# Kernel tuning notes

Measured on AMD Instinct MI355X. Metric: run time of the kernel, lower is better.

## Reference

```python
import jax, jax.numpy as jnp
import numpy as np

B, S, D = 1, 2048, 2048
H, HD = 32, 64  # num_heads, head_dim = hidden_size // num_heads


def setup_inputs() -> dict:
    key = jax.random.key(0)
    ks = jax.random.split(key, 7)
    sc = 0.02
    return {
        "hidden_states": jax.random.normal(ks[0], (B, S, D), dtype=jnp.float32),
        "Wq": jax.random.normal(ks[1], (D, D), dtype=jnp.float32) * sc,
        "Wk": jax.random.normal(ks[2], (D, D), dtype=jnp.float32) * sc,
        "Wv": jax.random.normal(ks[3], (D, D), dtype=jnp.float32) * sc,
        "Wf": jax.random.normal(ks[4], (H, D), dtype=jnp.float32) * sc,
        "bf": jax.random.normal(ks[5], (H,), dtype=jnp.float32),
        "Wo": jax.random.normal(ks[6], (D, D), dtype=jnp.float32) * sc,
    }


def reference(hidden_states, Wq, Wk, Wv, Wf, bf, Wo):
    x = hidden_states
    b, s, _ = x.shape
    # projections (nn.Linear: x @ W^T)
    q = (x @ Wq.T).reshape(b, s, H, HD)
    k = (x @ Wk.T).reshape(b, s, H, HD)
    v = (x @ Wv.T).reshape(b, s, H, HD)
    # per-head log forget gates, computed in float32 as in the torch module
    f = jax.nn.log_sigmoid((x @ Wf.T + bf).astype(jnp.float32))  # [b, s, H]
    # cumulative log decay; FoX bias D_ij = F_i - F_j (sum of log gates over (j, i])
    Fcum = jnp.cumsum(f, axis=1)               # [b, s, H]
    Fh = jnp.transpose(Fcum, (0, 2, 1))        # [b, H, s]
    scale = HD ** -0.5
    scores = jnp.einsum('bqhd,bkhd->bhqk', q, k).astype(jnp.float32) * scale
    scores = scores + Fh[:, :, :, None] - Fh[:, :, None, :]
    causal = jnp.tril(jnp.ones((s, s), dtype=bool))
    scores = jnp.where(causal[None, None], scores, -jnp.inf)
    p = jax.nn.softmax(scores, axis=-1).astype(q.dtype)  # [b, H, q, k]
    o = jnp.einsum('bhqk,bkhd->bqhd', p, v).reshape(b, s, D)
    return o @ Wo.T
```

## Files before the change

### kernel.cpp

```cpp
#include <hip/hip_runtime.h>
#include <stdint.h>

#define SEQ 2048
#define DM  2048
#define NH  32
#define HDIM 64

typedef unsigned short u16;
typedef short bf16x8 __attribute__((ext_vector_type(8)));
typedef float f32x4 __attribute__((ext_vector_type(4)));

__device__ __forceinline__ u16 f2bf(float f) {
    union { float f; uint32_t u; } v; v.f = f;
    uint32_t u = v.u;
    uint32_t r = (u + 0x7fffu + ((u >> 16) & 1u)) >> 16;
    return (u16)r;
}

#define GLOAD_LDS16(g, l) __builtin_amdgcn_global_load_lds( \
    (const __attribute__((address_space(1))) uint32_t*)(g), \
    (__attribute__((address_space(3))) uint32_t*)(l), 16, 0, 0)

__global__ __launch_bounds__(256) void convert_bf16(
    const float* __restrict__ X, const float* __restrict__ Wq,
    const float* __restrict__ Wk, const float* __restrict__ Wv,
    const float* __restrict__ Wo,
    u16* __restrict__ Xb, u16* __restrict__ Wqb, u16* __restrict__ Wkb,
    u16* __restrict__ Wvb, u16* __restrict__ Wob)
{
    const int NV = (DM * SEQ) / 4;
    int idx = blockIdx.x * blockDim.x + threadIdx.x;
    int total = NV * 5;
    for (; idx < total; idx += gridDim.x * blockDim.x) {
        int arr = idx / NV, i = idx - arr * NV;
        const float4* s; u16* d;
        switch (arr) {
            case 0:  s = (const float4*)X;  d = Xb;  break;
            case 1:  s = (const float4*)Wq; d = Wqb; break;
            case 2:  s = (const float4*)Wk; d = Wkb; break;
            case 3:  s = (const float4*)Wv; d = Wvb; break;
            default: s = (const float4*)Wo; d = Wob; break;
        }
        float4 v = s[i];
        ushort4 o;
        o.x = f2bf(v.x); o.y = f2bf(v.y); o.z = f2bf(v.z); o.w = f2bf(v.w);
        *(ushort4*)(d + i * 4) = o;
    }
}

__global__ __launch_bounds__(256) void gates_kernel(
    const float* __restrict__ X, const float* __restrict__ Wf,
    float* __restrict__ Fraw)
{
    __shared__ float lX[64 * 68];
    __shared__ float lW[32 * 68];
    int s0 = blockIdx.x * 64;
    int kp = blockIdx.y;
    int tid = threadIdx.x;
    int h = tid & 31, sg = tid >> 5;
    float acc[8] = {0.f,0.f,0.f,0.f,0.f,0.f,0.f,0.f};
    for (int k0 = kp * 512; k0 < kp * 512 + 512; k0 += 64) {
        __syncthreads();
        {
            int r = tid >> 2, seg = tid & 3;
            const float4* src = (const float4*)(X + (size_t)(s0 + r) * DM + k0);
            float4* dst = (float4*)(&lX[r * 68]);
#pragma unroll
            for (int i = 0; i < 4; i++) dst[seg + 4 * i] = src[seg + 4 * i];
#pragma unroll
            for (int j = 0; j < 2; j++) {
                int ii = tid + j * 256;
                int wr_ = ii >> 4, wc_ = ii & 15;
                ((float4*)(&lW[wr_ * 68]))[wc_] =
                    ((const float4*)(Wf + (size_t)wr_ * DM + k0))[wc_];
            }
        }
        __syncthreads();
#pragma unroll
        for (int k4 = 0; k4 < 16; k4++) {
            float4 w = ((const float4*)(&lW[h * 68]))[k4];
#pragma unroll
            for (int i = 0; i < 8; i++) {
                float4 x = ((const float4*)(&lX[(sg + 8 * i) * 68]))[k4];
                acc[i] += x.x * w.x + x.y * w.y + x.z * w.z + x.w * w.w;
            }
        }
    }
#pragma unroll
    for (int i = 0; i < 8; i++)
        atomicAdd(&Fraw[h * SEQ + s0 + sg + 8 * i], acc[i]);
}

__global__ __launch_bounds__(256) void cumsum_kernel(
    float* __restrict__ F, const float* __restrict__ bfp)
{
    __shared__ float lws[4];
    int h = blockIdx.x;
    int tid = threadIdx.x;
    int lane = tid & 63, wv = tid >> 6;
    float bb = bfp[h];
    float4 a = ((const float4*)(F + (size_t)h * SEQ))[tid * 2];
    float4 b2 = ((const float4*)(F + (size_t)h * SEQ))[tid * 2 + 1];
    float v[8] = {a.x, a.y, a.z, a.w, b2.x, b2.y, b2.z, b2.w};
#pragma unroll
    for (int i = 0; i < 8; i++) {
        float g = v[i] + bb;
        v[i] = fminf(g, 0.f) - log1pf(expf(-fabsf(g)));
    }
#pragma unroll
    for (int i = 1; i < 8; i++) v[i] += v[i - 1];
    float tsum = v[7];
    float sc = tsum;
#pragma unroll
    for (int d = 1; d < 64; d <<= 1) {
        float t = __shfl_up(sc, d);
        if (lane >= d) sc += t;
    }
    if (lane == 63) lws[wv] = sc;
    __syncthreads();
    float woff = 0.f;
#pragma unroll
    for (int w2 = 0; w2 < 4; w2++) if (w2 < wv) woff += lws[w2];
    float off = woff + sc - tsum;
#pragma unroll
    for (int i = 0; i < 8; i++) v[i] += off;
    float4 o1 = {v[0], v[1], v[2], v[3]}, o2 = {v[4], v[5], v[6], v[7]};
    ((float4*)(F + (size_t)h * SEQ))[tid * 2] = o1;
    ((float4*)(F + (size_t)h * SEQ))[tid * 2 + 1] = o2;
}

template <bool STOREF32>
__global__ __launch_bounds__(256) void gemm_bt(
    const u16* __restrict__ A,
    const u16* __restrict__ B0, const u16* __restrict__ B1, const u16* __restrict__ B2,
    void* C0, void* C1, void* C2, int M, int N, int K)
{
    __shared__ u16 lA[128 * 32];
    __shared__ u16 lB[128 * 32];
    int z = blockIdx.z;
    const u16* Bm = (z == 0) ? B0 : ((z == 1) ? B1 : B2);
    void* Cm = (z == 0) ? C0 : ((z == 1) ? C1 : C2);
    int m0 = blockIdx.y * 128, n0 = blockIdx.x * 128;
    int tid = threadIdx.x;
    int wave = tid >> 6, lane = tid & 63, ln = lane & 15, quad = lane >> 4;
    int wr = (wave >> 1) * 64, wc = (wave & 1) * 64;

    f32x4 acc[4][4];
#pragma unroll
    for (int i = 0; i < 4; i++)
#pragma unroll
        for (int j = 0; j < 4; j++)
#pragma unroll
            for (int r = 0; r < 4; r++) acc[i][j][r] = 0.f;

    int srow = wave * 32 + (lane >> 2);
    int scol = (lane & 3) * 8;
    const u16* gA0 = &A[(size_t)(m0 + srow) * K + scol];
    const u16* gA1 = &A[(size_t)(m0 + srow + 16) * K + scol];
    const u16* gB0 = &Bm[(size_t)(n0 + srow) * K + scol];
    const u16* gB1 = &Bm[(size_t)(n0 + srow + 16) * K + scol];
    u16* dA0 = &lA[(wave * 32) * 32];
    u16* dA1 = &lA[(wave * 32 + 16) * 32];
    u16* dB0 = &lB[(wave * 32) * 32];
    u16* dB1 = &lB[(wave * 32 + 16) * 32];

    for (int k0 = 0; k0 < K; k0 += 32) {
        __syncthreads();
        GLOAD_LDS16(gA0 + k0, dA0);
        GLOAD_LDS16(gA1 + k0, dA1);
        GLOAD_LDS16(gB0 + k0, dB0);
        GLOAD_LDS16(gB1 + k0, dB1);
        __syncthreads();
        bf16x8 af[4], bfr[4];
#pragma unroll
        for (int i = 0; i < 4; i++) af[i]  = *(const bf16x8*)(&lA[(wr + i * 16 + ln) * 32 + quad * 8]);
#pragma unroll
        for (int j = 0; j < 4; j++) bfr[j] = *(const bf16x8*)(&lB[(wc + j * 16 + ln) * 32 + quad * 8]);
#pragma unroll
        for (int i = 0; i < 4; i++)
#pragma unroll
            for (int j = 0; j < 4; j++)
                acc[i][j] = __builtin_amdgcn_mfma_f32_16x16x32_bf16(af[i], bfr[j], acc[i][j], 0, 0, 0);
    }

#pragma unroll
    for (int i = 0; i < 4; i++) {
#pragma unroll
        for (int j = 0; j < 4; j++) {
#pragma unroll
            for (int r = 0; r < 4; r++) {
                int row = m0 + wr + i * 16 + quad * 4 + r;
                int col = n0 + wc + j * 16 + ln;
                float v = acc[i][j][r];
                if (STOREF32) ((float*)Cm)[(size_t)row * N + col] = v;
                else          ((u16*)Cm)[(size_t)row * N + col]   = f2bf(v);
            }
        }
    }
}

__global__ __launch_bounds__(256) void attn_kernel(
    const u16* __restrict__ Q, const u16* __restrict__ K,
    const u16* __restrict__ V, const float* __restrict__ F,
    u16* __restrict__ O)
{
    __shared__ u16 lK[64 * 72];
    __shared__ u16 lV[64 * 72];
    __shared__ u16 lP[4 * 16 * 72];
    __shared__ float lFq[64];
    __shared__ float lFk[64];

    int h = blockIdx.y;
    int q0 = blockIdx.x * 64;
    int tid = threadIdx.x;
    int wave = tid >> 6, lane = tid & 63, ln = lane & 15, quad = lane >> 4;
    const float scale = 0.125f;

    bf16x8 aq[2];
    int qrow = q0 + wave * 16 + ln;
#pragma unroll
    for (int kk = 0; kk < 2; kk++)
        aq[kk] = *(const bf16x8*)(&Q[(size_t)qrow * DM + h * HDIM + kk * 32 + quad * 8]);

    if (tid < 64) lFq[tid] = F[h * SEQ + q0 + tid];

    float m_run[4], l_run[4];
    f32x4 o_acc[4];
#pragma unroll
    for (int r = 0; r < 4; r++) { m_run[r] = -1e30f; l_run[r] = 0.f; }
#pragma unroll
    for (int jo = 0; jo < 4; jo++)
#pragma unroll
        for (int r = 0; r < 4; r++) o_acc[jo][r] = 0.f;

    float Fq0 = F[h * SEQ + q0];
    int nt = q0 / 64 + 1;
    u16* lPw = &lP[wave * 16 * 72];

    for (int kt = 0; kt < nt; kt++) {
        int kb = kt * 64;
        if (kt < nt - 1) {
            float Fkend = F[h * SEQ + kb + 63];
            if (Fq0 - Fkend < -50.f) continue;
        }
        __syncthreads();
        {
            int row = tid >> 3, seg = tid & 7;
            *(uint4*)(&lK[row * 72 + seg * 8])        = *(const uint4*)(&K[(size_t)(kb + row) * DM + h * HDIM + seg * 8]);
            *(uint4*)(&lK[(row + 32) * 72 + seg * 8]) = *(const uint4*)(&K[(size_t)(kb + row + 32) * DM + h * HDIM + seg * 8]);
        }
#pragma unroll
        for (int half = 0; half < 2; half++) {
            int job = half * 256 + tid;
            int kv = job & 63, hs = job >> 6;
            union { uint4 v; u16 e[8]; } tmp;
            tmp.v = *(const uint4*)(&V[(size_t)(kb + kv) * DM + h * HDIM + hs * 8]);
#pragma unroll
            for (int u = 0; u < 8; u++) lV[(hs * 8 + u) * 72 + kv] = tmp.e[u];
        }
        if (tid < 64) lFk[tid] = F[h * SEQ + kb + tid];
        __syncthreads();

        f32x4 s_acc[4];
#pragma unroll
        for (int j = 0; j < 4; j++)
#pragma unroll
            for (int r = 0; r < 4; r++) s_acc[j][r] = 0.f;
#pragma unroll
        for (int kk = 0; kk < 2; kk++)
#pragma unroll
            for (int j = 0; j < 4; j++) {
                bf16x8 bk = *(const bf16x8*)(&lK[(j * 16 + ln) * 72 + kk * 32 + quad * 8]);
                s_acc[j] = __builtin_amdgcn_mfma_f32_16x16x32_bf16(aq[kk], bk, s_acc[j], 0, 0, 0);
            }

        bool diag = (kt == nt - 1);
        int qbase = q0 + wave * 16 + quad * 4;
        float vv[4][4];
        float m_new[4];
#pragma unroll
        for (int r = 0; r < 4; r++) m_new[r] = -1e30f;
#pragma unroll
        for (int j = 0; j < 4; j++) {
            float fk = lFk[j * 16 + ln];
            int kglob = kb + j * 16 + ln;
#pragma unroll
            for (int r = 0; r < 4; r++) {
                float fq = lFq[wave * 16 + quad * 4 + r];
                float v = s_acc[j][r] * scale + (fq - fk);
                if (diag && kglob > qbase + r) v = -1e30f;
                vv[j][r] = v;
                m_new[r] = fmaxf(m_new[r], v);
            }
        }
#pragma unroll
        for (int r = 0; r < 4; r++) {
#pragma unroll
            for (int m = 1; m < 16; m <<= 1) m_new[r] = fmaxf(m_new[r], __shfl_xor(m_new[r], m));
        }
        float alpha[4];
#pragma unroll
        for (int r = 0; r < 4; r++) {
            float mt = fmaxf(m_run[r], m_new[r]);
            alpha[r] = expf(m_run[r] - mt);
            m_run[r] = mt;
        }
        float lsum[4] = {0.f, 0.f, 0.f, 0.f};
#pragma unroll
        for (int j = 0; j < 4; j++)
#pragma unroll
            for (int r = 0; r < 4; r++) {
                float pv = expf(vv[j][r] - m_run[r]);
                vv[j][r] = pv;
                lsum[r] += pv;
            }
#pragma unroll
        for (int r = 0; r < 4; r++) {
#pragma unroll
            for (int m = 1; m < 16; m <<= 1) lsum[r] += __shfl_xor(lsum[r], m);
            l_run[r] = l_run[r] * alpha[r] + lsum[r];
        }
#pragma unroll
        for (int jo = 0; jo < 4; jo++)
#pragma unroll
            for (int r = 0; r < 4; r++) o_acc[jo][r] *= alpha[r];

#pragma unroll
        for (int j = 0; j < 4; j++)
#pragma unroll
            for (int r = 0; r < 4; r++)
                lPw[(quad * 4 + r) * 72 + j * 16 + ln] = f2bf(vv[j][r]);
        __syncthreads();
        bf16x8 ap[2];
#pragma unroll
        for (int kk = 0; kk < 2; kk++)
            ap[kk] = *(const bf16x8*)(&lPw[ln * 72 + kk * 32 + quad * 8]);
#pragma unroll
        for (int kk = 0; kk < 2; kk++)
#pragma unroll
            for (int jo = 0; jo < 4; jo++) {
                bf16x8 bv = *(const bf16x8*)(&lV[(jo * 16 + ln) * 72 + kk * 32 + quad * 8]);
                o_acc[jo] = __builtin_amdgcn_mfma_f32_16x16x32_bf16(ap[kk], bv, o_acc[jo], 0, 0, 0);
            }
    }

#pragma unroll
    for (int r = 0; r < 4; r++) {
        float inv = 1.f / l_run[r];
        int row = q0 + wave * 16 + quad * 4 + r;
#pragma unroll
        for (int jo = 0; jo < 4; jo++)
            O[(size_t)row * DM + h * HDIM + jo * 16 + ln] = f2bf(o_acc[jo][r] * inv);
    }
}

extern "C" void kernel_launch(void* const* d_in, const int* in_sizes, int n_in,
                              void* d_out, int out_size, void* d_ws, size_t ws_size,
                              hipStream_t stream)
{
    const float* X   = (const float*)d_in[0];
    const float* Wq  = (const float*)d_in[1];
    const float* Wk  = (const float*)d_in[2];
    const float* Wv  = (const float*)d_in[3];
    const float* Wf  = (const float*)d_in[4];
    const float* bfp = (const float*)d_in[5];
    const float* Wo  = (const float*)d_in[6];
    float* out = (float*)d_out;

    char* ws = (char*)d_ws;
    const size_t MB8 = (size_t)DM * SEQ * 2;
    u16* Xb  = (u16*)(ws + 0 * MB8);
    u16* Wqb = (u16*)(ws + 1 * MB8);
    u16* Wkb = (u16*)(ws + 2 * MB8);
    u16* Wvb = (u16*)(ws + 3 * MB8);
    u16* Wob = (u16*)(ws + 4 * MB8);
    u16* Qb  = (u16*)(ws + 5 * MB8);
    u16* Kb  = (u16*)(ws + 6 * MB8);
    u16* Vb  = (u16*)(ws + 7 * MB8);
    u16* Ob  = (u16*)(ws + 8 * MB8);
    float* Fb = (float*)(ws + 9 * MB8);

    hipMemsetAsync(Fb, 0, (size_t)NH * SEQ * sizeof(float), stream);
    convert_bf16<<<dim3(4096), dim3(256), 0, stream>>>(X, Wq, Wk, Wv, Wo, Xb, Wqb, Wkb, Wvb, Wob);
    gates_kernel<<<dim3(32, 4), dim3(256), 0, stream>>>(X, Wf, Fb);
    cumsum_kernel<<<dim3(NH), dim3(256), 0, stream>>>(Fb, bfp);
    gemm_bt<false><<<dim3(16, 16, 3), dim3(256), 0, stream>>>(
        Xb, Wqb, Wkb, Wvb, (void*)Qb, (void*)Kb, (void*)Vb, SEQ, DM, DM);
    attn_kernel<<<dim3(SEQ / 64, NH), dim3(256), 0, stream>>>(Qb, Kb, Vb, Fb, Ob);
    gemm_bt<true><<<dim3(16, 16, 1), dim3(256), 0, stream>>>(
        Ob, Wob, Wob, Wob, (void*)out, (void*)out, (void*)out, SEQ, DM, DM);
}
```

Baseline: 333.0 us.

## Specialize GEMMs, drop memset and atomics in gates, add launch bounds

The templated GEMM is split into separate QKV and output kernels with compile-time K/N and pointer-increment loads. Occupancy hints are added through launch_bounds (3 for the GEMMs, 2 for attention). The gates kernel now walks the full K range in one block per row tile and stores directly. This removes the memset and the atomics, at the cost of fewer blocks (32) doing a serial K loop.

```diff
diff --git a/kernel.cpp b/kernel.cpp
--- a/kernel.cpp
+++ b/kernel.cpp
@@ -21,7 +21,7 @@
     (const __attribute__((address_space(1))) uint32_t*)(g), \
     (__attribute__((address_space(3))) uint32_t*)(l), 16, 0, 0)
 
-__global__ __launch_bounds__(256) void convert_bf16(
+__global__ __launch_bounds__(256) void cvt_bf16(
     const float* __restrict__ X, const float* __restrict__ Wq,
     const float* __restrict__ Wk, const float* __restrict__ Wv,
     const float* __restrict__ Wo,
@@ -48,18 +48,17 @@
     }
 }
 
-__global__ __launch_bounds__(256) void gates_kernel(
+__global__ __launch_bounds__(256) void gates_gemm(
     const float* __restrict__ X, const float* __restrict__ Wf,
     float* __restrict__ Fraw)
 {
     __shared__ float lX[64 * 68];
     __shared__ float lW[32 * 68];
     int s0 = blockIdx.x * 64;
-    int kp = blockIdx.y;
     int tid = threadIdx.x;
     int h = tid & 31, sg = tid >> 5;
     float acc[8] = {0.f,0.f,0.f,0.f,0.f,0.f,0.f,0.f};
-    for (int k0 = kp * 512; k0 < kp * 512 + 512; k0 += 64) {
+    for (int k0 = 0; k0 < DM; k0 += 64) {
         __syncthreads();
         {
             int r = tid >> 2, seg = tid & 3;
@@ -88,10 +87,10 @@
     }
 #pragma unroll
     for (int i = 0; i < 8; i++)
-        atomicAdd(&Fraw[h * SEQ + s0 + sg + 8 * i], acc[i]);
-}
-
-__global__ __launch_bounds__(256) void cumsum_kernel(
+        Fraw[h * SEQ + s0 + sg + 8 * i] = acc[i];
+}
+
+__global__ __launch_bounds__(256) void gates_scan(
     float* __restrict__ F, const float* __restrict__ bfp)
 {
     __shared__ float lws[4];
@@ -129,17 +128,17 @@
     ((float4*)(F + (size_t)h * SEQ))[tid * 2 + 1] = o2;
 }
 
-template <bool STOREF32>
-__global__ __launch_bounds__(256) void gemm_bt(
+__global__ __launch_bounds__(256, 3) void gemm_qkv(
     const u16* __restrict__ A,
     const u16* __restrict__ B0, const u16* __restrict__ B1, const u16* __restrict__ B2,
-    void* C0, void* C1, void* C2, int M, int N, int K)
+    u16* __restrict__ C0, u16* __restrict__ C1, u16* __restrict__ C2)
 {
     __shared__ u16 lA[128 * 32];
     __shared__ u16 lB[128 * 32];
+    const int K = DM, N = DM;
     int z = blockIdx.z;
     const u16* Bm = (z == 0) ? B0 : ((z == 1) ? B1 : B2);
-    void* Cm = (z == 0) ? C0 : ((z == 1) ? C1 : C2);
+    u16* Cm = (z == 0) ? C0 : ((z == 1) ? C1 : C2);
     int m0 = blockIdx.y * 128, n0 = blockIdx.x * 128;
     int tid = threadIdx.x;
     int wave = tid >> 6, lane = tid & 63, ln = lane & 15, quad = lane >> 4;
@@ -164,12 +163,13 @@
     u16* dB0 = &lB[(wave * 32) * 32];
     u16* dB1 = &lB[(wave * 32 + 16) * 32];
 
-    for (int k0 = 0; k0 < K; k0 += 32) {
-        __syncthreads();
-        GLOAD_LDS16(gA0 + k0, dA0);
-        GLOAD_LDS16(gA1 + k0, dA1);
-        GLOAD_LDS16(gB0 + k0, dB0);
-        GLOAD_LDS16(gB1 + k0, dB1);
+    for (int kk0 = 0; kk0 < K / 32; kk0++) {
+        __syncthreads();
+        GLOAD_LDS16(gA0, dA0);
+        GLOAD_LDS16(gA1, dA1);
+        GLOAD_LDS16(gB0, dB0);
+        GLOAD_LDS16(gB1, dB1);
+        gA0 += 32; gA1 += 32; gB0 += 32; gB1 += 32;
         __syncthreads();
         bf16x8 af[4], bfr[4];
 #pragma unroll
@@ -184,22 +184,81 @@
     }
 
 #pragma unroll
-    for (int i = 0; i < 4; i++) {
-#pragma unroll
-        for (int j = 0; j < 4; j++) {
+    for (int i = 0; i < 4; i++)
+#pragma unroll
+        for (int j = 0; j < 4; j++)
 #pragma unroll
             for (int r = 0; r < 4; r++) {
                 int row = m0 + wr + i * 16 + quad * 4 + r;
                 int col = n0 + wc + j * 16 + ln;
-                float v = acc[i][j][r];
-                if (STOREF32) ((float*)Cm)[(size_t)row * N + col] = v;
-                else          ((u16*)Cm)[(size_t)row * N + col]   = f2bf(v);
-            }
-        }
-    }
-}
-
-__global__ __launch_bounds__(256) void attn_kernel(
+                Cm[(size_t)row * N + col] = f2bf(acc[i][j][r]);
+            }
+}
+
+__global__ __launch_bounds__(256, 3) void gemm_out(
+    const u16* __restrict__ A, const u16* __restrict__ B,
+    float* __restrict__ C)
+{
+    __shared__ u16 lA[128 * 32];
+    __shared__ u16 lB[128 * 32];
+    const int K = DM, N = DM;
+    int m0 = blockIdx.y * 128, n0 = blockIdx.x * 128;
+    int tid = threadIdx.x;
+    int wave = tid >> 6, lane = tid & 63, ln = lane & 15, quad = lane >> 4;
+    int wr = (wave >> 1) * 64, wc = (wave & 1) * 64;
+
+    f32x4 acc[4][4];
+#pragma unroll
+    for (int i = 0; i < 4; i++)
+#pragma unroll
+        for (int j = 0; j < 4; j++)
+#pragma unroll
+            for (int r = 0; r < 4; r++) acc[i][j][r] = 0.f;
+
+    int srow = wave * 32 + (lane >> 2);
+    int scol = (lane & 3) * 8;
+    const u16* gA0 = &A[(size_t)(m0 + srow) * K + scol];
+    const u16* gA1 = &A[(size_t)(m0 + srow + 16) * K + scol];
+    const u16* gB0 = &B[(size_t)(n0 + srow) * K + scol];
+    const u16* gB1 = &B[(size_t)(n0 + srow + 16) * K + scol];
+    u16* dA0 = &lA[(wave * 32) * 32];
+    u16* dA1 = &lA[(wave * 32 + 16) * 32];
+    u16* dB0 = &lB[(wave * 32) * 32];
+    u16* dB1 = &lB[(wave * 32 + 16) * 32];
+
+    for (int kk0 = 0; kk0 < K / 32; kk0++) {
+        __syncthreads();
+        GLOAD_LDS16(gA0, dA0);
+        GLOAD_LDS16(gA1, dA1);
+        GLOAD_LDS16(gB0, dB0);
+        GLOAD_LDS16(gB1, dB1);
+        gA0 += 32; gA1 += 32; gB0 += 32; gB1 += 32;
+        __syncthreads();
+        bf16x8 af[4], bfr[4];
+#pragma unroll
+        for (int i = 0; i < 4; i++) af[i]  = *(const bf16x8*)(&lA[(wr + i * 16 + ln) * 32 + quad * 8]);
+#pragma unroll
+        for (int j = 0; j < 4; j++) bfr[j] = *(const bf16x8*)(&lB[(wc + j * 16 + ln) * 32 + quad * 8]);
+#pragma unroll
+        for (int i = 0; i < 4; i++)
+#pragma unroll
+            for (int j = 0; j < 4; j++)
+                acc[i][j] = __builtin_amdgcn_mfma_f32_16x16x32_bf16(af[i], bfr[j], acc[i][j], 0, 0, 0);
+    }
+
+#pragma unroll
+    for (int i = 0; i < 4; i++)
+#pragma unroll
+        for (int j = 0; j < 4; j++)
+#pragma unroll
+            for (int r = 0; r < 4; r++) {
+                int row = m0 + wr + i * 16 + quad * 4 + r;
+                int col = n0 + wc + j * 16 + ln;
+                C[(size_t)row * N + col] = acc[i][j][r];
+            }
+}
+
+__global__ __launch_bounds__(256, 2) void attn_fox(
     const u16* __restrict__ Q, const u16* __restrict__ K,
     const u16* __restrict__ V, const float* __restrict__ F,
     u16* __restrict__ O)
@@ -380,13 +439,10 @@
     u16* Ob  = (u16*)(ws + 8 * MB8);
     float* Fb = (float*)(ws + 9 * MB8);
 
-    hipMemsetAsync(Fb, 0, (size_t)NH * SEQ * sizeof(float), stream);
-    convert_bf16<<<dim3(4096), dim3(256), 0, stream>>>(X, Wq, Wk, Wv, Wo, Xb, Wqb, Wkb, Wvb, Wob);
-    gates_kernel<<<dim3(32, 4), dim3(256), 0, stream>>>(X, Wf, Fb);
-    cumsum_kernel<<<dim3(NH), dim3(256), 0, stream>>>(Fb, bfp);
-    gemm_bt<false><<<dim3(16, 16, 3), dim3(256), 0, stream>>>(
-        Xb, Wqb, Wkb, Wvb, (void*)Qb, (void*)Kb, (void*)Vb, SEQ, DM, DM);
-    attn_kernel<<<dim3(SEQ / 64, NH), dim3(256), 0, stream>>>(Qb, Kb, Vb, Fb, Ob);
-    gemm_bt<true><<<dim3(16, 16, 1), dim3(256), 0, stream>>>(
-        Ob, Wob, Wob, Wob, (void*)out, (void*)out, (void*)out, SEQ, DM, DM);
-}
+    cvt_bf16<<<dim3(4096), dim3(256), 0, stream>>>(X, Wq, Wk, Wv, Wo, Xb, Wqb, Wkb, Wvb, Wob);
+    gates_gemm<<<dim3(32), dim3(256), 0, stream>>>(X, Wf, Fb);
+    gates_scan<<<dim3(NH), dim3(256), 0, stream>>>(Fb, bfp);
+    gemm_qkv<<<dim3(16, 16, 3), dim3(256), 0, stream>>>(Xb, Wqb, Wkb, Wvb, Qb, Kb, Vb);
+    attn_fox<<<dim3(SEQ / 64, NH), dim3(256), 0, stream>>>(Qb, Kb, Vb, Fb, Ob);
+    gemm_out<<<dim3(16, 16), dim3(256), 0, stream>>>(Ob, Wob, out);
+}
```

After: 396.1 us. 18.9% more time.
